# Kernel optimization log

Hardware: AMD Instinct MI355X
Metric: run time of the kernel (lower is better)

## Reference

```python
import jax, jax.numpy as jnp
import numpy as np

B, NV, FD = 16, 128, 8192
T_TEMP = 0.2      # self.T
MARGIN = 1.0      # nn.TripletMarginLoss default
EPS = 1e-6        # pairwise_distance eps


def _l2norm(x):
    # torch F.normalize(dim=1): x / max(||x||, 1e-12)
    nrm = jnp.maximum(jnp.linalg.norm(x, axis=-1, keepdims=True), 1e-12)
    return x / nrm


def _ssl_parts(qb, kb, nb, num_gt):
    # qb,kb,nb: [NV, FD] flattened reid embeddings for one image
    qv = _l2norm(qb)[:num_gt]          # [g, FD]
    kv = _l2norm(kb)[:num_gt]          # [g, FD]
    nv = _l2norm(nb)                   # [NV, FD] (negatives are NOT sliced)
    g = num_gt
    S = qv @ kv.T                      # [g, g] all pairwise dots (replaces torch.dot loops)
    # similarity-matrix loss
    sm = jnp.sum((S - jnp.eye(g, dtype=S.dtype)) ** 2) / (g * g)
    # pairwise distances with torch eps convention: ||a - b + eps||_2
    # = sqrt(||a||^2 + ||b||^2 - 2 a.b + 2*eps*(sum(a)-sum(b)) + D*eps^2); ||a||=||b||=1
    sq = qv.sum(axis=1)                # [g]
    sk = kv.sum(axis=1)                # [g]
    const = FD * EPS * EPS
    d_qk = jnp.sqrt(jnp.maximum(2.0 - 2.0 * S + 2.0 * EPS * (sq[:, None] - sk[None, :]) + const, 0.0))
    d_kq = jnp.sqrt(jnp.maximum(2.0 - 2.0 * S.T + 2.0 * EPS * (sk[:, None] - sq[None, :]) + const, 0.0))
    off = 1.0 - jnp.eye(g, dtype=S.dtype)
    # triplet: anc=q_i,pos=k_i,neg=k_j  and  anc=k_i,pos=q_i,neg=q_j, j != i
    tri1 = jnp.sum(jax.nn.relu(jnp.diag(d_qk)[:, None] - d_qk + MARGIN) * off)
    tri2 = jnp.sum(jax.nn.relu(jnp.diag(d_kq)[:, None] - d_kq + MARGIN) * off)
    tri_sum = tri1 + tri2
    # cycle consistency: |q_i.k_j - k_i.q_j| = |S[i,j] - S[j,i]|
    cyc = jnp.sum(jnp.abs(S - S.T) * off) / (g * (g - 1))
    # InfoNCE: l_pos = q_i.k_i, l_neg = q @ n.T
    l_pos = jnp.diag(S)[:, None]       # [g, 1]
    l_neg = qv @ nv.T                  # [g, NV]
    logits = jnp.concatenate([l_pos, l_neg], axis=1) / T_TEMP
    ce = jnp.mean(jax.nn.logsumexp(logits, axis=1) - logits[:, 0])  # CE with labels=0
    return sm, tri_sum, cyc, ce / g


def setup_inputs() -> dict:
    key = jax.random.key(0)
    kq, kk, kn = jax.random.split(key, 3)
    q = jax.random.normal(kq, (B, NV, FD), dtype=jnp.float32)
    k = jax.random.normal(kk, (B, NV, FD), dtype=jnp.float32)
    n = jax.random.normal(kn, (B, NV, FD), dtype=jnp.float32)
    return {"q": q, "k": k, "n": n, "num_gt": NV}


def reference(q, k, n, num_gt):
    sm, tri, cyc, ce = jax.vmap(lambda a, b, c: _ssl_parts(a, b, c, num_gt))(q, k, n)
    tri_cnt = 2 * num_gt * (num_gt - 1)
    # original bug: tri_loss accumulates across batches while tri_cnt resets,
    # so each batch contributes cumsum(tri)[b] / tri_cnt
    ssl = jnp.sum(sm) + jnp.sum(jnp.cumsum(tri)) / tri_cnt + jnp.sum(cyc) + jnp.sum(ce)
    return ssl
```

## Files before the change

kernel.cpp:

```cpp
#include <hip/hip_runtime.h>
#include <cstdint>
#include <cstddef>

#define B_N   16
#define G_N   128
#define FD_N  8192
#define BK    64

typedef unsigned short u16;
typedef u16  u16x4 __attribute__((ext_vector_type(4)));
typedef u16  u16x8 __attribute__((ext_vector_type(8)));
typedef __bf16 bf16x8 __attribute__((ext_vector_type(8)));
typedef float f32x16 __attribute__((ext_vector_type(16)));

#define STATS_SSQ_Q 0
#define STATS_SUM_Q 2048
#define STATS_SSQ_K 4096
#define STATS_SUM_K 6144
#define STATS_SSQ_N 8192
#define SM_ACC      10240
#define CE_ACC      12288
#define ZERO_FLOATS 14336
#define S_OFF       14336
#define PART_OFF    276480

__device__ __forceinline__ u16 f2bf(float f) {
    uint32_t u = __float_as_uint(f);
    u += 0x7FFFu + ((u >> 16) & 1u);
    return (u16)(u >> 16);
}

#define LDS_BARRIER() asm volatile("s_waitcnt lgkmcnt(0)\n\ts_barrier" ::: "memory")

__global__ __launch_bounds__(512, 4)
void k_gemm(const float* __restrict__ q, const float* __restrict__ kM,
            const float* __restrict__ nM, float* __restrict__ ws,
            int ksplit, int kc)
{
    __shared__ __align__(16) u16 sA[G_N * BK];
    __shared__ __align__(16) u16 sB[G_N * BK];

    const int tid = threadIdx.x;
    const int blk = blockIdx.x;
    const int b    = blk / (2 * ksplit);
    const int rem  = blk - b * 2 * ksplit;
    const int half = rem / ksplit;
    const int kch  = rem - half * ksplit;
    const int niter = kc / BK;

    const size_t mat_off = (size_t)b * G_N * FD_N + (size_t)kch * kc + (size_t)(tid & 15) * 4;
    const float* Ap = q + mat_off;
    const float* Bp = (half ? nM : kM) + mat_off;
    const int r0 = tid >> 4;
    const int c4 = tid & 15;

    float4 la[4], lb[4];
    float aS[4] = {0,0,0,0}, aQ[4] = {0,0,0,0};
    float bS[4] = {0,0,0,0}, bQ[4] = {0,0,0,0};

    #pragma unroll
    for (int i = 0; i < 4; ++i) la[i] = *(const float4*)(Ap + (size_t)(r0 + 32*i) * FD_N);
    #pragma unroll
    for (int i = 0; i < 4; ++i) lb[i] = *(const float4*)(Bp + (size_t)(r0 + 32*i) * FD_N);

    const int lane  = tid & 63;
    const int wv    = tid >> 6;
    const int wm    = wv >> 2;
    const int wn    = wv & 3;
    const int khalf = lane >> 5;
    const int lrow  = lane & 31;

    f32x16 acc[2];
    #pragma unroll
    for (int mb = 0; mb < 2; ++mb)
      #pragma unroll
      for (int e = 0; e < 16; ++e) acc[mb][e] = 0.f;

    const int rA0 = wm*64 + lrow;
    const int rB0 = wn*32 + lrow;

    for (int kb = 0; kb < niter; ++kb) {
        LDS_BARRIER();
        #pragma unroll
        for (int i = 0; i < 4; ++i) {
            float4 v = la[i];
            aS[i] += v.x + v.y + v.z + v.w;
            aQ[i] += v.x*v.x + v.y*v.y + v.z*v.z + v.w*v.w;
            u16x4 h; h[0]=f2bf(v.x); h[1]=f2bf(v.y); h[2]=f2bf(v.z); h[3]=f2bf(v.w);
            int row = r0 + 32*i;
            *(u16x4*)(sA + row*BK + (((c4>>1) ^ (row&7))<<3) + ((c4&1)<<2)) = h;
        }
        #pragma unroll
        for (int i = 0; i < 4; ++i) {
            float4 v = lb[i];
            bS[i] += v.x + v.y + v.z + v.w;
            bQ[i] += v.x*v.x + v.y*v.y + v.z*v.z + v.w*v.w;
            u16x4 h; h[0]=f2bf(v.x); h[1]=f2bf(v.y); h[2]=f2bf(v.z); h[3]=f2bf(v.w);
            int row = r0 + 32*i;
            *(u16x4*)(sB + row*BK + (((c4>>1) ^ (row&7))<<3) + ((c4&1)<<2)) = h;
        }
        LDS_BARRIER();
        if (kb + 1 < niter) {
            const float* An = Ap + (kb+1)*BK;
            const float* Bn = Bp + (kb+1)*BK;
            #pragma unroll
            for (int i = 0; i < 4; ++i) la[i] = *(const float4*)(An + (size_t)(r0 + 32*i) * FD_N);
            #pragma unroll
            for (int i = 0; i < 4; ++i) lb[i] = *(const float4*)(Bn + (size_t)(r0 + 32*i) * FD_N);
        }
        #pragma unroll
        for (int s = 0; s < 4; ++s) {
            int chunk = s*2 + khalf;
            bf16x8 af[2], bf;
            #pragma unroll
            for (int mb = 0; mb < 2; ++mb) {
                int row = rA0 + mb*32;
                u16x8 raw = *(const u16x8*)(sA + row*BK + ((chunk ^ (row&7))<<3));
                af[mb] = __builtin_bit_cast(bf16x8, raw);
            }
            {
                int row = rB0;
                u16x8 raw = *(const u16x8*)(sB + row*BK + ((chunk ^ (row&7))<<3));
                bf = __builtin_bit_cast(bf16x8, raw);
            }
            #pragma unroll
            for (int mb = 0; mb < 2; ++mb)
                acc[mb] = __builtin_amdgcn_mfma_f32_32x32x16_bf16(af[mb], bf, acc[mb], 0, 0, 0);
        }
    }

    float* part = ws + PART_OFF + (size_t)blk * (G_N * G_N);
    #pragma unroll
    for (int mb = 0; mb < 2; ++mb) {
        int col = wn*32 + lrow;
        int rbase = wm*64 + mb*32 + 4*khalf;
        #pragma unroll
        for (int reg = 0; reg < 16; ++reg) {
            int row = rbase + (reg & 3) + 8*(reg >> 2);
            part[(size_t)row * G_N + col] = acc[mb][reg];
        }
    }

    #pragma unroll
    for (int i = 0; i < 4; ++i) {
        float sa = aS[i], qa = aQ[i], sb = bS[i], qb = bQ[i];
        for (int m = 8; m >= 1; m >>= 1) {
            sa += __shfl_xor(sa, m, 64); qa += __shfl_xor(qa, m, 64);
            sb += __shfl_xor(sb, m, 64); qb += __shfl_xor(qb, m, 64);
        }
        if ((lane & 15) == 0) {
            int row = r0 + 32*i;
            if (half == 0) {
                atomicAdd(ws + STATS_SUM_Q + b*G_N + row, sa);
                atomicAdd(ws + STATS_SSQ_Q + b*G_N + row, qa);
                atomicAdd(ws + STATS_SUM_K + b*G_N + row, sb);
                atomicAdd(ws + STATS_SSQ_K + b*G_N + row, qb);
            } else {
                atomicAdd(ws + STATS_SSQ_N + b*G_N + row, qb);
            }
        }
    }
}

__global__ __launch_bounds__(256)
void k_red2(float* __restrict__ ws, int ksplit)
{
    const int idx  = blockIdx.x * 256 + threadIdx.x;
    const int col4 = idx & 31;
    const int i    = (idx >> 5) & 127;
    const int half = (idx >> 12) & 1;
    const int b    = idx >> 13;

    const float4* base = (const float4*)(ws + PART_OFF)
                       + ((size_t)((b*2 + half) * ksplit)) * 4096 + i*32 + col4;
    float4 s = {0.f, 0.f, 0.f, 0.f};
    for (int kch = 0; kch < ksplit; ++kch) {
        float4 v = base[(size_t)kch * 4096];
        s.x += v.x; s.y += v.y; s.z += v.z; s.w += v.w;
    }

    const float iq = 1.f / fmaxf(sqrtf(ws[STATS_SSQ_Q + b*G_N + i]), 1e-12f);

    if (half == 0) {
        float4 kss = *(const float4*)(ws + STATS_SSQ_K + b*G_N + col4*4);
        float4 S4;
        S4.x = s.x * iq / fmaxf(sqrtf(kss.x), 1e-12f);
        S4.y = s.y * iq / fmaxf(sqrtf(kss.y), 1e-12f);
        S4.z = s.z * iq / fmaxf(sqrtf(kss.z), 1e-12f);
        S4.w = s.w * iq / fmaxf(sqrtf(kss.w), 1e-12f);
        ((float4*)(ws + S_OFF))[(size_t)b*4096 + i*32 + col4] = S4;
        int j0 = col4*4;
        float d0 = S4.x - (j0+0 == i ? 1.f : 0.f);
        float d1 = S4.y - (j0+1 == i ? 1.f : 0.f);
        float d2 = S4.z - (j0+2 == i ? 1.f : 0.f);
        float d3 = S4.w - (j0+3 == i ? 1.f : 0.f);
        float sm = d0*d0 + d1*d1 + d2*d2 + d3*d3;
        for (int m = 16; m >= 1; m >>= 1) sm += __shfl_xor(sm, m, 64);
        if (col4 == 0) atomicAdd(ws + SM_ACC + b*G_N + i, sm);
    } else {
        float4 nss = *(const float4*)(ws + STATS_SSQ_N + b*G_N + col4*4);
        float e = __expf(s.x * iq / fmaxf(sqrtf(nss.x), 1e-12f) * 5.0f)
                + __expf(s.y * iq / fmaxf(sqrtf(nss.y), 1e-12f) * 5.0f)
                + __expf(s.z * iq / fmaxf(sqrtf(nss.z), 1e-12f) * 5.0f)
                + __expf(s.w * iq / fmaxf(sqrtf(nss.w), 1e-12f) * 5.0f);
        for (int m = 16; m >= 1; m >>= 1) e += __shfl_xor(e, m, 64);
        if (col4 == 0) atomicAdd(ws + CE_ACC + b*G_N + i, e);
    }
}

__global__ __launch_bounds__(256)
void k_epi(float* __restrict__ ws, float* __restrict__ out)
{
    const int b     = blockIdx.x >> 3;
    const int chunk = blockIdx.x & 7;
    const int i0    = chunk * 16;
    const int t     = threadIdx.x;
    __shared__ float sqv_s[128], skv_s[128], ddq_s[128], ddk_s[128];
    __shared__ float rbuf[4];

    const float c0 = (float)FD_N * 1e-6f * 1e-6f;
    const float* S = ws + S_OFF + (size_t)b * 16384;

    if (t < 128) {
        float iq = 1.f / fmaxf(sqrtf(ws[STATS_SSQ_Q + b*G_N + t]), 1e-12f);
        float sq = ws[STATS_SUM_Q + b*G_N + t] * iq;
        float ik = 1.f / fmaxf(sqrtf(ws[STATS_SSQ_K + b*G_N + t]), 1e-12f);
        float sk = ws[STATS_SUM_K + b*G_N + t] * ik;
        sqv_s[t] = sq; skv_s[t] = sk;
        float S_tt = S[t*128 + t];
        ddq_s[t] = sqrtf(fmaxf(2.f - 2.f*S_tt + 2e-6f*(sq - sk) + c0, 0.f));
        ddk_s[t] = sqrtf(fmaxf(2.f - 2.f*S_tt + 2e-6f*(sk - sq) + c0, 0.f));
    }
    __syncthreads();

    float tri = 0.f, cyc = 0.f, ce = 0.f, sm = 0.f;
    for (int p = t; p < 2048; p += 256) {
        int i = i0 + (p >> 7), j = p & 127;
        if (i != j) {
            float S_ij = S[i*128 + j];
            float dqk = sqrtf(fmaxf(2.f - 2.f*S_ij + 2e-6f*(sqv_s[i]-skv_s[j]) + c0, 0.f));
            tri += fmaxf(ddq_s[i] - dqk + 1.f, 0.f);
            float dkq = sqrtf(fmaxf(2.f - 2.f*S_ij + 2e-6f*(skv_s[j]-sqv_s[i]) + c0, 0.f));
            tri += fmaxf(ddk_s[j] - dkq + 1.f, 0.f);
            cyc += fabsf(S_ij - S[j*128 + i]);
        }
    }
    if (t < 16) {
        int r = i0 + t;
        float lp = 5.f * S[r*128 + r];
        ce = __logf(ws[CE_ACC + b*G_N + r] + __expf(lp)) - lp;
    }
    if (chunk == 0 && t < 128) sm = ws[SM_ACC + b*G_N + t];

    float contrib = sm / 16384.f + cyc / 16256.f + ce / 16384.f
                  + (float)(B_N - b) * tri / 32512.f;
    for (int m = 32; m >= 1; m >>= 1) contrib += __shfl_xor(contrib, m, 64);
    int wvi = t >> 6, ln0 = t & 63;
    if (ln0 == 0) rbuf[wvi] = contrib;
    __syncthreads();
    if (t == 0) atomicAdd(out, rbuf[0] + rbuf[1] + rbuf[2] + rbuf[3]);
}

extern "C" void kernel_launch(void* const* d_in, const int* in_sizes, int n_in,
                              void* d_out, int out_size, void* d_ws, size_t ws_size,
                              hipStream_t stream)
{
    const float* q  = (const float*)d_in[0];
    const float* kM = (const float*)d_in[1];
    const float* nM = (const float*)d_in[2];
    float* ws  = (float*)d_ws;
    float* out = (float*)d_out;

    int ksplit = 16;
    while (ksplit > 1 &&
           ((size_t)PART_OFF + (size_t)(B_N * 2 * ksplit) * (G_N * G_N)) * sizeof(float) > ws_size)
        ksplit >>= 1;
    int kc = FD_N / ksplit;

    hipMemsetAsync(d_ws, 0, ZERO_FLOATS * sizeof(float), stream);
    hipMemsetAsync(d_out, 0, sizeof(float), stream);
    k_gemm<<<B_N * 2 * ksplit, 512, 0, stream>>>(q, kM, nM, ws, ksplit, kc);
    k_red2<<<512, 256, 0, stream>>>(ws, ksplit);
    k_epi<<<B_N * 8, 256, 0, stream>>>(ws, out);
}
```

Measured before the change: 231.7 us.

## Rework split-K GEMM pipeline with bf16 partials, deterministic stats, no memsets

Hardcodes a 16-way K split and halves the k-step to 32 with a two-stage register prefetch of global loads. Partial GEMM tiles are now stored as bf16 instead of fp32, which halves the workspace traffic between the GEMM and the reduce kernel. Per-row statistics, similarity-matrix and CE accumulators are written per chunk and summed later instead of using atomics, so both memsets are removed. A small final kernel replaces the output atomic. Rounding partials to bf16 costs accuracy, and the hardcoded split drops the workspace-size fallback.

```diff
diff --git a/kernel.cpp b/kernel.cpp
--- a/kernel.cpp
+++ b/kernel.cpp
@@ -5,7 +5,10 @@
 #define B_N   16
 #define G_N   128
 #define FD_N  8192
-#define BK    64
+#define KSPLIT 16
+#define KC    512
+#define BK2   32
+#define NITER 16
 
 typedef unsigned short u16;
 typedef u16  u16x4 __attribute__((ext_vector_type(4)));
@@ -13,16 +16,16 @@
 typedef __bf16 bf16x8 __attribute__((ext_vector_type(8)));
 typedef float f32x16 __attribute__((ext_vector_type(16)));
 
-#define STATS_SSQ_Q 0
-#define STATS_SUM_Q 2048
-#define STATS_SSQ_K 4096
-#define STATS_SUM_K 6144
-#define STATS_SSQ_N 8192
-#define SM_ACC      10240
-#define CE_ACC      12288
-#define ZERO_FLOATS 14336
-#define S_OFF       14336
-#define PART_OFF    276480
+#define QSUM_P   0
+#define QSSQ_P   32768
+#define KSUM_P   65536
+#define KSSQ_P   98304
+#define NSSQ_P   131072
+#define SM_ROW   163840
+#define CE_ROW   165888
+#define S_OFF    167936
+#define CONTRIB  430080
+#define PART_OFF_F 430208
 
 __device__ __forceinline__ u16 f2bf(float f) {
     uint32_t u = __float_as_uint(f);
@@ -34,34 +37,38 @@
 
 __global__ __launch_bounds__(512, 4)
 void k_gemm(const float* __restrict__ q, const float* __restrict__ kM,
-            const float* __restrict__ nM, float* __restrict__ ws,
-            int ksplit, int kc)
-{
-    __shared__ __align__(16) u16 sA[G_N * BK];
-    __shared__ __align__(16) u16 sB[G_N * BK];
+            const float* __restrict__ nM, float* __restrict__ ws)
+{
+    __shared__ __align__(16) u16 sA[G_N * BK2];
+    __shared__ __align__(16) u16 sB[G_N * BK2];
 
     const int tid = threadIdx.x;
     const int blk = blockIdx.x;
-    const int b    = blk / (2 * ksplit);
-    const int rem  = blk - b * 2 * ksplit;
-    const int half = rem / ksplit;
-    const int kch  = rem - half * ksplit;
-    const int niter = kc / BK;
-
-    const size_t mat_off = (size_t)b * G_N * FD_N + (size_t)kch * kc + (size_t)(tid & 15) * 4;
+    const int b    = blk >> 5;
+    const int rem  = blk & 31;
+    const int half = rem >> 4;
+    const int kch  = rem & 15;
+
+    const int r0 = tid >> 3;
+    const int c8 = tid & 7;
+
+    const size_t mat_off = (size_t)b * (G_N * FD_N) + (size_t)kch * KC + (size_t)(c8 * 4);
     const float* Ap = q + mat_off;
     const float* Bp = (half ? nM : kM) + mat_off;
-    const int r0 = tid >> 4;
-    const int c4 = tid & 15;
-
-    float4 la[4], lb[4];
-    float aS[4] = {0,0,0,0}, aQ[4] = {0,0,0,0};
-    float bS[4] = {0,0,0,0}, bQ[4] = {0,0,0,0};
-
-    #pragma unroll
-    for (int i = 0; i < 4; ++i) la[i] = *(const float4*)(Ap + (size_t)(r0 + 32*i) * FD_N);
-    #pragma unroll
-    for (int i = 0; i < 4; ++i) lb[i] = *(const float4*)(Bp + (size_t)(r0 + 32*i) * FD_N);
+
+    float4 la[2][2], lb[2][2];
+    float aS[2] = {0,0}, aQ[2] = {0,0}, bS[2] = {0,0}, bQ[2] = {0,0};
+
+    #pragma unroll
+    for (int st = 0; st < 2; ++st) {
+        const float* A2 = Ap + st * BK2;
+        const float* B2 = Bp + st * BK2;
+        #pragma unroll
+        for (int i = 0; i < 2; ++i) {
+            la[st][i] = *(const float4*)(A2 + (size_t)(r0 + 64*i) * FD_N);
+            lb[st][i] = *(const float4*)(B2 + (size_t)(r0 + 64*i) * FD_N);
+        }
+    }
 
     const int lane  = tid & 63;
     const int wv    = tid >> 6;
@@ -69,6 +76,8 @@
     const int wn    = wv & 3;
     const int khalf = lane >> 5;
     const int lrow  = lane & 31;
+    const int rA0 = wm*64 + lrow;
+    const int rB0 = wn*32 + lrow;
 
     f32x16 acc[2];
     #pragma unroll
@@ -76,60 +85,52 @@
       #pragma unroll
       for (int e = 0; e < 16; ++e) acc[mb][e] = 0.f;
 
-    const int rA0 = wm*64 + lrow;
-    const int rB0 = wn*32 + lrow;
-
-    for (int kb = 0; kb < niter; ++kb) {
+    for (int kb = 0; kb < NITER; ++kb) {
+        const int st = kb & 1;
         LDS_BARRIER();
         #pragma unroll
-        for (int i = 0; i < 4; ++i) {
-            float4 v = la[i];
+        for (int i = 0; i < 2; ++i) {
+            int row = r0 + 64*i;
+            int wof = row*BK2 + (((c8>>1) ^ (row&3))<<3) + ((c8&1)<<2);
+            float4 v = la[st][i];
             aS[i] += v.x + v.y + v.z + v.w;
             aQ[i] += v.x*v.x + v.y*v.y + v.z*v.z + v.w*v.w;
             u16x4 h; h[0]=f2bf(v.x); h[1]=f2bf(v.y); h[2]=f2bf(v.z); h[3]=f2bf(v.w);
-            int row = r0 + 32*i;
-            *(u16x4*)(sA + row*BK + (((c4>>1) ^ (row&7))<<3) + ((c4&1)<<2)) = h;
-        }
-        #pragma unroll
-        for (int i = 0; i < 4; ++i) {
-            float4 v = lb[i];
+            *(u16x4*)(sA + wof) = h;
+            v = lb[st][i];
             bS[i] += v.x + v.y + v.z + v.w;
             bQ[i] += v.x*v.x + v.y*v.y + v.z*v.z + v.w*v.w;
-            u16x4 h; h[0]=f2bf(v.x); h[1]=f2bf(v.y); h[2]=f2bf(v.z); h[3]=f2bf(v.w);
-            int row = r0 + 32*i;
-            *(u16x4*)(sB + row*BK + (((c4>>1) ^ (row&7))<<3) + ((c4&1)<<2)) = h;
+            u16x4 h2; h2[0]=f2bf(v.x); h2[1]=f2bf(v.y); h2[2]=f2bf(v.z); h2[3]=f2bf(v.w);
+            *(u16x4*)(sB + wof) = h2;
         }
         LDS_BARRIER();
-        if (kb + 1 < niter) {
-            const float* An = Ap + (kb+1)*BK;
-            const float* Bn = Bp + (kb+1)*BK;
+        if (kb + 2 < NITER) {
+            const float* A2 = Ap + (kb+2) * BK2;
+            const float* B2 = Bp + (kb+2) * BK2;
             #pragma unroll
-            for (int i = 0; i < 4; ++i) la[i] = *(const float4*)(An + (size_t)(r0 + 32*i) * FD_N);
-            #pragma unroll
-            for (int i = 0; i < 4; ++i) lb[i] = *(const float4*)(Bn + (size_t)(r0 + 32*i) * FD_N);
-        }
-        #pragma unroll
-        for (int s = 0; s < 4; ++s) {
+            for (int i = 0; i < 2; ++i) {
+                la[st][i] = *(const float4*)(A2 + (size_t)(r0 + 64*i) * FD_N);
+                lb[st][i] = *(const float4*)(B2 + (size_t)(r0 + 64*i) * FD_N);
+            }
+        }
+        #pragma unroll
+        for (int s = 0; s < 2; ++s) {
             int chunk = s*2 + khalf;
-            bf16x8 af[2], bf;
+            bf16x8 af[2], bfv;
             #pragma unroll
             for (int mb = 0; mb < 2; ++mb) {
                 int row = rA0 + mb*32;
-                u16x8 raw = *(const u16x8*)(sA + row*BK + ((chunk ^ (row&7))<<3));
+                u16x8 raw = *(const u16x8*)(sA + row*BK2 + ((chunk ^ (row&3))<<3));
                 af[mb] = __builtin_bit_cast(bf16x8, raw);
             }
-            {
-                int row = rB0;
-                u16x8 raw = *(const u16x8*)(sB + row*BK + ((chunk ^ (row&7))<<3));
-                bf = __builtin_bit_cast(bf16x8, raw);
-            }
-            #pragma unroll
-            for (int mb = 0; mb < 2; ++mb)
-                acc[mb] = __builtin_amdgcn_mfma_f32_32x32x16_bf16(af[mb], bf, acc[mb], 0, 0, 0);
-        }
-    }
-
-    float* part = ws + PART_OFF + (size_t)blk * (G_N * G_N);
+            u16x8 rawb = *(const u16x8*)(sB + rB0*BK2 + ((chunk ^ (rB0&3))<<3));
+            bfv = __builtin_bit_cast(bf16x8, rawb);
+            acc[0] = __builtin_amdgcn_mfma_f32_32x32x16_bf16(af[0], bfv, acc[0], 0, 0, 0);
+            acc[1] = __builtin_amdgcn_mfma_f32_32x32x16_bf16(af[1], bfv, acc[1], 0, 0, 0);
+        }
+    }
+
+    u16* part = (u16*)(ws + PART_OFF_F) + ((size_t)blk << 14);
     #pragma unroll
     for (int mb = 0; mb < 2; ++mb) {
         int col = wn*32 + lrow;
@@ -137,128 +138,167 @@
         #pragma unroll
         for (int reg = 0; reg < 16; ++reg) {
             int row = rbase + (reg & 3) + 8*(reg >> 2);
-            part[(size_t)row * G_N + col] = acc[mb][reg];
-        }
-    }
-
-    #pragma unroll
-    for (int i = 0; i < 4; ++i) {
+            part[row*G_N + col] = f2bf(acc[mb][reg]);
+        }
+    }
+
+    #pragma unroll
+    for (int i = 0; i < 2; ++i) {
         float sa = aS[i], qa = aQ[i], sb = bS[i], qb = bQ[i];
-        for (int m = 8; m >= 1; m >>= 1) {
+        #pragma unroll
+        for (int m = 4; m >= 1; m >>= 1) {
             sa += __shfl_xor(sa, m, 64); qa += __shfl_xor(qa, m, 64);
             sb += __shfl_xor(sb, m, 64); qb += __shfl_xor(qb, m, 64);
         }
-        if ((lane & 15) == 0) {
-            int row = r0 + 32*i;
+        if (c8 == 0) {
+            int o = kch*2048 + b*G_N + (r0 + 64*i);
             if (half == 0) {
-                atomicAdd(ws + STATS_SUM_Q + b*G_N + row, sa);
-                atomicAdd(ws + STATS_SSQ_Q + b*G_N + row, qa);
-                atomicAdd(ws + STATS_SUM_K + b*G_N + row, sb);
-                atomicAdd(ws + STATS_SSQ_K + b*G_N + row, qb);
+                ws[QSUM_P + o] = sa; ws[QSSQ_P + o] = qa;
+                ws[KSUM_P + o] = sb; ws[KSSQ_P + o] = qb;
             } else {
-                atomicAdd(ws + STATS_SSQ_N + b*G_N + row, qb);
+                ws[NSSQ_P + o] = qb;
             }
         }
     }
 }
 
 __global__ __launch_bounds__(256)
-void k_red2(float* __restrict__ ws, int ksplit)
-{
-    const int idx  = blockIdx.x * 256 + threadIdx.x;
-    const int col4 = idx & 31;
-    const int i    = (idx >> 5) & 127;
-    const int half = (idx >> 12) & 1;
-    const int b    = idx >> 13;
-
-    const float4* base = (const float4*)(ws + PART_OFF)
-                       + ((size_t)((b*2 + half) * ksplit)) * 4096 + i*32 + col4;
-    float4 s = {0.f, 0.f, 0.f, 0.f};
-    for (int kch = 0; kch < ksplit; ++kch) {
-        float4 v = base[(size_t)kch * 4096];
-        s.x += v.x; s.y += v.y; s.z += v.z; s.w += v.w;
-    }
-
-    const float iq = 1.f / fmaxf(sqrtf(ws[STATS_SSQ_Q + b*G_N + i]), 1e-12f);
-
+void k_red2(float* __restrict__ ws)
+{
+    const int blk  = blockIdx.x;
+    const int b    = blk >> 4;
+    const int half = (blk >> 3) & 1;
+    const int rg   = blk & 7;
+    const int t    = threadIdx.x;
+    const int lr   = t >> 4;
+    const int i    = rg*16 + lr;
+    const int c8   = t & 15;
+    __shared__ float nrm[128];
+    __shared__ float invq_s[16];
+
+    if (t < 128) {
+        float ss = 0.f;
+        const float* p = ws + (half ? NSSQ_P : KSSQ_P) + b*G_N + t;
+        #pragma unroll
+        for (int kc2 = 0; kc2 < KSPLIT; ++kc2) ss += p[kc2*2048];
+        nrm[t] = 1.f / fmaxf(sqrtf(ss), 1e-12f);
+    } else if (t < 144) {
+        float ss = 0.f;
+        const float* p = ws + QSSQ_P + b*G_N + rg*16 + (t - 128);
+        #pragma unroll
+        for (int kc2 = 0; kc2 < KSPLIT; ++kc2) ss += p[kc2*2048];
+        invq_s[t-128] = 1.f / fmaxf(sqrtf(ss), 1e-12f);
+    }
+    __syncthreads();
+
+    const u16* part = (const u16*)(ws + PART_OFF_F);
+    float s[8] = {0,0,0,0,0,0,0,0};
+    #pragma unroll
+    for (int kc2 = 0; kc2 < KSPLIT; ++kc2) {
+        size_t idx = ((size_t)(b*32 + half*16 + kc2) << 14) + i*G_N + c8*8;
+        u16x8 h = *(const u16x8*)(part + idx);
+        #pragma unroll
+        for (int e = 0; e < 8; ++e)
+            s[e] += __uint_as_float(((uint32_t)h[e]) << 16);
+    }
+    const float iq = invq_s[lr];
     if (half == 0) {
-        float4 kss = *(const float4*)(ws + STATS_SSQ_K + b*G_N + col4*4);
-        float4 S4;
-        S4.x = s.x * iq / fmaxf(sqrtf(kss.x), 1e-12f);
-        S4.y = s.y * iq / fmaxf(sqrtf(kss.y), 1e-12f);
-        S4.z = s.z * iq / fmaxf(sqrtf(kss.z), 1e-12f);
-        S4.w = s.w * iq / fmaxf(sqrtf(kss.w), 1e-12f);
-        ((float4*)(ws + S_OFF))[(size_t)b*4096 + i*32 + col4] = S4;
-        int j0 = col4*4;
-        float d0 = S4.x - (j0+0 == i ? 1.f : 0.f);
-        float d1 = S4.y - (j0+1 == i ? 1.f : 0.f);
-        float d2 = S4.z - (j0+2 == i ? 1.f : 0.f);
-        float d3 = S4.w - (j0+3 == i ? 1.f : 0.f);
-        float sm = d0*d0 + d1*d1 + d2*d2 + d3*d3;
-        for (int m = 16; m >= 1; m >>= 1) sm += __shfl_xor(sm, m, 64);
-        if (col4 == 0) atomicAdd(ws + SM_ACC + b*G_N + i, sm);
+        float smacc = 0.f;
+        float S8[8];
+        #pragma unroll
+        for (int e = 0; e < 8; ++e) {
+            int j = c8*8 + e;
+            S8[e] = s[e] * iq * nrm[j];
+            float d = S8[e] - (j == i ? 1.f : 0.f);
+            smacc += d*d;
+        }
+        float* Sp = ws + S_OFF + (size_t)b*16384 + i*G_N + c8*8;
+        float4 w0 = {S8[0],S8[1],S8[2],S8[3]};
+        float4 w1 = {S8[4],S8[5],S8[6],S8[7]};
+        *(float4*)Sp = w0; *(float4*)(Sp+4) = w1;
+        #pragma unroll
+        for (int m = 8; m >= 1; m >>= 1) smacc += __shfl_xor(smacc, m, 64);
+        if (c8 == 0) ws[SM_ROW + b*G_N + i] = smacc;
     } else {
-        float4 nss = *(const float4*)(ws + STATS_SSQ_N + b*G_N + col4*4);
-        float e = __expf(s.x * iq / fmaxf(sqrtf(nss.x), 1e-12f) * 5.0f)
-                + __expf(s.y * iq / fmaxf(sqrtf(nss.y), 1e-12f) * 5.0f)
-                + __expf(s.z * iq / fmaxf(sqrtf(nss.z), 1e-12f) * 5.0f)
-                + __expf(s.w * iq / fmaxf(sqrtf(nss.w), 1e-12f) * 5.0f);
-        for (int m = 16; m >= 1; m >>= 1) e += __shfl_xor(e, m, 64);
-        if (col4 == 0) atomicAdd(ws + CE_ACC + b*G_N + i, e);
+        float eacc = 0.f;
+        #pragma unroll
+        for (int e = 0; e < 8; ++e)
+            eacc += __expf(5.f * s[e] * iq * nrm[c8*8+e]);
+        #pragma unroll
+        for (int m = 8; m >= 1; m >>= 1) eacc += __shfl_xor(eacc, m, 64);
+        if (c8 == 0) ws[CE_ROW + b*G_N + i] = eacc;
     }
 }
 
 __global__ __launch_bounds__(256)
-void k_epi(float* __restrict__ ws, float* __restrict__ out)
-{
-    const int b     = blockIdx.x >> 3;
-    const int chunk = blockIdx.x & 7;
-    const int i0    = chunk * 16;
-    const int t     = threadIdx.x;
-    __shared__ float sqv_s[128], skv_s[128], ddq_s[128], ddk_s[128];
+void k_epi(float* __restrict__ ws)
+{
+    const int blk = blockIdx.x;
+    const int b   = blk >> 3;
+    const int i0  = (blk & 7) * 16;
+    const int t   = threadIdx.x;
+    __shared__ float sqv[128], skv[128], ddq[128], ddk[128];
     __shared__ float rbuf[4];
-
     const float c0 = (float)FD_N * 1e-6f * 1e-6f;
+
     const float* S = ws + S_OFF + (size_t)b * 16384;
-
     if (t < 128) {
-        float iq = 1.f / fmaxf(sqrtf(ws[STATS_SSQ_Q + b*G_N + t]), 1e-12f);
-        float sq = ws[STATS_SUM_Q + b*G_N + t] * iq;
-        float ik = 1.f / fmaxf(sqrtf(ws[STATS_SSQ_K + b*G_N + t]), 1e-12f);
-        float sk = ws[STATS_SUM_K + b*G_N + t] * ik;
-        sqv_s[t] = sq; skv_s[t] = sk;
-        float S_tt = S[t*128 + t];
-        ddq_s[t] = sqrtf(fmaxf(2.f - 2.f*S_tt + 2e-6f*(sq - sk) + c0, 0.f));
-        ddk_s[t] = sqrtf(fmaxf(2.f - 2.f*S_tt + 2e-6f*(sk - sq) + c0, 0.f));
+        float qs=0, qq=0, ks=0, kq=0;
+        #pragma unroll
+        for (int kc2 = 0; kc2 < KSPLIT; ++kc2) {
+            int o = kc2*2048 + b*G_N + t;
+            qs += ws[QSUM_P + o]; qq += ws[QSSQ_P + o];
+            ks += ws[KSUM_P + o]; kq += ws[KSSQ_P + o];
+        }
+        float iq = 1.f/fmaxf(sqrtf(qq),1e-12f);
+        float ik = 1.f/fmaxf(sqrtf(kq),1e-12f);
+        float sq = qs*iq, sk = ks*ik;
+        sqv[t]=sq; skv[t]=sk;
+        float Stt = S[t*G_N + t];
+        ddq[t] = sqrtf(fmaxf(2.f - 2.f*Stt + 2e-6f*(sq-sk) + c0, 0.f));
+        ddk[t] = sqrtf(fmaxf(2.f - 2.f*Stt + 2e-6f*(sk-sq) + c0, 0.f));
     }
     __syncthreads();
 
-    float tri = 0.f, cyc = 0.f, ce = 0.f, sm = 0.f;
-    for (int p = t; p < 2048; p += 256) {
-        int i = i0 + (p >> 7), j = p & 127;
+    float tri=0.f, cyc=0.f, ce=0.f, sm=0.f;
+    #pragma unroll
+    for (int p = 0; p < 8; ++p) {
+        int idx = p*256 + t;
+        int i = i0 + (idx >> 7), j = idx & 127;
         if (i != j) {
-            float S_ij = S[i*128 + j];
-            float dqk = sqrtf(fmaxf(2.f - 2.f*S_ij + 2e-6f*(sqv_s[i]-skv_s[j]) + c0, 0.f));
-            tri += fmaxf(ddq_s[i] - dqk + 1.f, 0.f);
-            float dkq = sqrtf(fmaxf(2.f - 2.f*S_ij + 2e-6f*(skv_s[j]-sqv_s[i]) + c0, 0.f));
-            tri += fmaxf(ddk_s[j] - dkq + 1.f, 0.f);
-            cyc += fabsf(S_ij - S[j*128 + i]);
+            float S_ij = S[i*G_N + j];
+            float dqk = sqrtf(fmaxf(2.f - 2.f*S_ij + 2e-6f*(sqv[i]-skv[j]) + c0, 0.f));
+            tri += fmaxf(ddq[i] - dqk + 1.f, 0.f);
+            float dkq = sqrtf(fmaxf(2.f - 2.f*S_ij + 2e-6f*(skv[j]-sqv[i]) + c0, 0.f));
+            tri += fmaxf(ddk[j] - dkq + 1.f, 0.f);
+            cyc += fabsf(S_ij - S[j*G_N + i]);
         }
     }
     if (t < 16) {
         int r = i0 + t;
-        float lp = 5.f * S[r*128 + r];
-        ce = __logf(ws[CE_ACC + b*G_N + r] + __expf(lp)) - lp;
-    }
-    if (chunk == 0 && t < 128) sm = ws[SM_ACC + b*G_N + t];
-
-    float contrib = sm / 16384.f + cyc / 16256.f + ce / 16384.f
-                  + (float)(B_N - b) * tri / 32512.f;
+        float lp = 5.f * S[r*G_N + r];
+        ce = __logf(ws[CE_ROW + b*G_N + r] + __expf(lp)) - lp;
+        sm = ws[SM_ROW + b*G_N + r];
+    }
+    float contrib = sm * (1.f/16384.f) + cyc * (1.f/16256.f) + ce * (1.f/16384.f)
+                  + (float)(B_N - b) * tri * (1.f/32512.f);
+    #pragma unroll
     for (int m = 32; m >= 1; m >>= 1) contrib += __shfl_xor(contrib, m, 64);
-    int wvi = t >> 6, ln0 = t & 63;
-    if (ln0 == 0) rbuf[wvi] = contrib;
+    if ((t & 63) == 0) rbuf[t >> 6] = contrib;
     __syncthreads();
-    if (t == 0) atomicAdd(out, rbuf[0] + rbuf[1] + rbuf[2] + rbuf[3]);
+    if (t == 0) ws[CONTRIB + blk] = rbuf[0] + rbuf[1] + rbuf[2] + rbuf[3];
+}
+
+__global__ void k_fin(const float* __restrict__ ws, float* __restrict__ out)
+{
+    __shared__ float r2[2];
+    int t = threadIdx.x;
+    float v = ws[CONTRIB + t];
+    #pragma unroll
+    for (int m = 32; m >= 1; m >>= 1) v += __shfl_xor(v, m, 64);
+    if ((t & 63) == 0) r2[t >> 6] = v;
+    __syncthreads();
+    if (t == 0) out[0] = r2[0] + r2[1];
 }
 
 extern "C" void kernel_launch(void* const* d_in, const int* in_sizes, int n_in,
@@ -271,15 +311,8 @@
     float* ws  = (float*)d_ws;
     float* out = (float*)d_out;
 
-    int ksplit = 16;
-    while (ksplit > 1 &&
-           ((size_t)PART_OFF + (size_t)(B_N * 2 * ksplit) * (G_N * G_N)) * sizeof(float) > ws_size)
-        ksplit >>= 1;
-    int kc = FD_N / ksplit;
-
-    hipMemsetAsync(d_ws, 0, ZERO_FLOATS * sizeof(float), stream);
-    hipMemsetAsync(d_out, 0, sizeof(float), stream);
-    k_gemm<<<B_N * 2 * ksplit, 512, 0, stream>>>(q, kM, nM, ws, ksplit, kc);
-    k_red2<<<512, 256, 0, stream>>>(ws, ksplit);
-    k_epi<<<B_N * 8, 256, 0, stream>>>(ws, out);
-}
+    k_gemm<<<B_N * 2 * KSPLIT, 512, 0, stream>>>(q, kM, nM, ws);
+    k_red2<<<256, 256, 0, stream>>>(ws);
+    k_epi<<<128, 256, 0, stream>>>(ws);
+    k_fin<<<1, 128, 0, stream>>>(ws, out);
+}
```

Measured after the change: 268.6 us. 15.9% more time.
